# Optimization experiments

Measured on AMD Instinct MI355X. Metric: run time of the kernel, lower is better.

## Reference

```python
import jax, jax.numpy as jnp
import numpy as np

_EPS = 1e-8

# Stacked Sobel kernels, pre-divided by 8 (matches conv2d(...)/8.0 in torch).
# Shape: (O=2, I=1, 3, 3); channel 0 = sobel_x, channel 1 = sobel_y.
_SOBEL = jnp.stack([
    jnp.array([[-1.0, 0.0, 1.0], [-2.0, 0.0, 2.0], [-1.0, 0.0, 1.0]], jnp.float32),
    jnp.array([[-1.0, -2.0, -1.0], [0.0, 0.0, 0.0], [1.0, 2.0, 1.0]], jnp.float32),
])[:, None, :, :] / 8.0


def setup_inputs() -> dict:
    key = jax.random.key(0)
    k1, k2 = jax.random.split(key)
    B, C, H, W = 64, 1, 512, 512
    pred_dist = jax.random.uniform(k1, (B, C, H, W), dtype=jnp.float32) * 10.0
    reachable = jax.random.uniform(k2, (B, C, H, W), dtype=jnp.float32)
    return {"pred_dist": pred_dist, "reachable": reachable}


def reference(pred_dist, reachable) -> jnp.ndarray:
    # Replicate (edge) padding, as F.pad(..., mode='replicate')
    padded = jnp.pad(pred_dist, ((0, 0), (0, 0), (1, 1), (1, 1)), mode="edge")
    # Single conv with 2 output channels computes grad_x and grad_y together.
    grads = jax.lax.conv_general_dilated(
        padded, _SOBEL.astype(pred_dist.dtype),
        window_strides=(1, 1), padding="VALID",
        dimension_numbers=("NCHW", "OIHW", "NCHW"),
    )  # [B, 2, H, W]
    gx = grads[:, 0:1]
    gy = grads[:, 1:2]
    magnitude = jnp.sqrt(gx * gx + gy * gy + _EPS)
    violation = jnp.abs(magnitude - 1.0)
    mask = (reachable > 0.5).astype(violation.dtype)
    denom = jnp.maximum(mask.sum(), 1.0)
    return (violation * mask).sum() / denom
```

## Files before the change

### kernel.cpp

```cpp
#include <hip/hip_runtime.h>
#include <math.h>

#define HW   512
#define IMG  (512 * 512)
#define NB   64
#define GROUPS_PER_ROW 128
#define TOTAL_GROUPS   (NB * HW * GROUPS_PER_ROW)
#define BLOCK 256
#define NBLOCKS 2048
#define NTHREADS (NBLOCKS * BLOCK)

__global__ __launch_bounds__(BLOCK) void eik_main(const float* __restrict__ pred,
                                                  const float* __restrict__ reach,
                                                  float* __restrict__ partials) {
    float vsum = 0.0f;
    float csum = 0.0f;

    for (int g = blockIdx.x * BLOCK + threadIdx.x; g < TOTAL_GROUPS; g += NTHREADS) {
        const int x0 = (g & (GROUPS_PER_ROW - 1)) << 2;
        const int y  = (g >> 7) & (HW - 1);
        const int b  = g >> 16;

        const float* base = pred + (size_t)b * IMG;
        const float* row0 = base + (size_t)y * HW;
        const float* rowm = base + (size_t)(y > 0      ? y - 1 : 0)      * HW;
        const float* rowp = base + (size_t)(y < HW - 1 ? y + 1 : HW - 1) * HW;

        const float4 cm = *(const float4*)(rowm + x0);
        const float4 c0 = *(const float4*)(row0 + x0);
        const float4 cp = *(const float4*)(rowp + x0);
        const float lm = (x0 == 0)        ? rowm[0]    : rowm[x0 - 1];
        const float l0 = (x0 == 0)        ? row0[0]    : row0[x0 - 1];
        const float lp = (x0 == 0)        ? rowp[0]    : rowp[x0 - 1];
        const float rm = (x0 == HW - 4)   ? rowm[HW-1] : rowm[x0 + 4];
        const float r0 = (x0 == HW - 4)   ? row0[HW-1] : row0[x0 + 4];
        const float rp = (x0 == HW - 4)   ? rowp[HW-1] : rowp[x0 + 4];

        const float wm[6] = {lm, cm.x, cm.y, cm.z, cm.w, rm};
        const float w0[6] = {l0, c0.x, c0.y, c0.z, c0.w, r0};
        const float wp[6] = {lp, cp.x, cp.y, cp.z, cp.w, rp};

        const float4 rch = *(const float4*)(reach + (size_t)b * IMG + (size_t)y * HW + x0);
        const float rv[4] = {rch.x, rch.y, rch.z, rch.w};

#pragma unroll
        for (int i = 0; i < 4; ++i) {
            const float gx = ((wm[i+2] - wm[i]) + 2.0f * (w0[i+2] - w0[i]) + (wp[i+2] - wp[i])) * 0.125f;
            const float gy = ((wp[i]   - wm[i]) + 2.0f * (wp[i+1] - wm[i+1]) + (wp[i+2] - wm[i+2])) * 0.125f;
            const float mag  = sqrtf(gx * gx + gy * gy + 1e-8f);
            const float viol = fabsf(mag - 1.0f);
            const bool  m    = rv[i] > 0.5f;
            vsum += m ? viol : 0.0f;
            csum += m ? 1.0f : 0.0f;
        }
    }

#pragma unroll
    for (int off = 32; off > 0; off >>= 1) {
        vsum += __shfl_down(vsum, off, 64);
        csum += __shfl_down(csum, off, 64);
    }

    __shared__ float sv[BLOCK / 64];
    __shared__ float sc[BLOCK / 64];
    const int lane = threadIdx.x & 63;
    const int wid  = threadIdx.x >> 6;
    if (lane == 0) { sv[wid] = vsum; sc[wid] = csum; }
    __syncthreads();
    if (threadIdx.x == 0) {
        partials[2 * blockIdx.x]     = sv[0] + sv[1] + sv[2] + sv[3];
        partials[2 * blockIdx.x + 1] = sc[0] + sc[1] + sc[2] + sc[3];
    }
}

__global__ __launch_bounds__(BLOCK) void eik_finalize(const float* __restrict__ partials,
                                                      float* __restrict__ out) {
    float v = 0.0f, c = 0.0f;
    for (int i = threadIdx.x; i < NBLOCKS; i += BLOCK) {
        v += partials[2 * i];
        c += partials[2 * i + 1];
    }
#pragma unroll
    for (int off = 32; off > 0; off >>= 1) {
        v += __shfl_down(v, off, 64);
        c += __shfl_down(c, off, 64);
    }
    __shared__ float sv[BLOCK / 64];
    __shared__ float sc[BLOCK / 64];
    const int lane = threadIdx.x & 63;
    const int wid  = threadIdx.x >> 6;
    if (lane == 0) { sv[wid] = v; sc[wid] = c; }
    __syncthreads();
    if (threadIdx.x == 0) {
        const float vt = sv[0] + sv[1] + sv[2] + sv[3];
        const float ct = sc[0] + sc[1] + sc[2] + sc[3];
        out[0] = vt / fmaxf(ct, 1.0f);
    }
}

extern "C" void kernel_launch(void* const* d_in, const int* in_sizes, int n_in,
                              void* d_out, int out_size, void* d_ws, size_t ws_size,
                              hipStream_t stream) {
    const float* pred  = (const float*)d_in[0];
    const float* reach = (const float*)d_in[1];
    float* out = (float*)d_out;
    float* ws  = (float*)d_ws;

    eik_main<<<NBLOCKS, BLOCK, 0, stream>>>(pred, reach, ws);
    eik_finalize<<<1, BLOCK, 0, stream>>>(ws, out);
}
```

Measured before the change: 150.6 us.

## Use wave-per-row-strip sliding window with shuffle halos for Sobel stencil

Each 64-lane wave now owns a full 512-wide row and walks down a strip of 8 rows. It keeps three row windows in registers and loads only one new row per step. Horizontal halo values come from lane shuffles instead of extra scalar global loads, which removes the redundant 3x row reloads and the 6 unaligned scalar loads per thread. In exchange, the grid becomes 1024 non-persistent blocks, and halo rows are reloaded at strip boundaries.

```diff
diff --git a/kernel.cpp b/kernel.cpp
--- a/kernel.cpp
+++ b/kernel.cpp
@@ -4,47 +4,64 @@
 #define HW   512
 #define IMG  (512 * 512)
 #define NB   64
-#define GROUPS_PER_ROW 128
-#define TOTAL_GROUPS   (NB * HW * GROUPS_PER_ROW)
+#define T    8
 #define BLOCK 256
-#define NBLOCKS 2048
-#define NTHREADS (NBLOCKS * BLOCK)
+#define WAVES_PER_IMG (HW / T)
+#define TOTAL_WAVES   (NB * WAVES_PER_IMG)
+#define NBLOCKS       (TOTAL_WAVES / (BLOCK / 64))
+
+__device__ __forceinline__ void load_row(const float* __restrict__ prow, int r, int lane,
+                                         float4& q0, float4& q1) {
+    const float* p = prow + (size_t)r * HW + (lane << 3);
+    q0 = *(const float4*)p;
+    q1 = *(const float4*)(p + 4);
+}
+
+__device__ __forceinline__ void make_window(const float4& q0, const float4& q1, int lane,
+                                            float* w) {
+    float lft = __shfl_up(q1.w, 1, 64);
+    float rgt = __shfl_down(q0.x, 1, 64);
+    if (lane == 0)  lft = q0.x;
+    if (lane == 63) rgt = q1.w;
+    w[0] = lft;  w[1] = q0.x; w[2] = q0.y; w[3] = q0.z; w[4] = q0.w;
+    w[5] = q1.x; w[6] = q1.y; w[7] = q1.z; w[8] = q1.w; w[9] = rgt;
+}
 
 __global__ __launch_bounds__(BLOCK) void eik_main(const float* __restrict__ pred,
                                                   const float* __restrict__ reach,
                                                   float* __restrict__ partials) {
-    float vsum = 0.0f;
-    float csum = 0.0f;
+    const int lane = threadIdx.x & 63;
+    const int wave = blockIdx.x * (BLOCK / 64) + (threadIdx.x >> 6);
+    const int b    = wave >> 6;
+    const int y0   = (wave & (WAVES_PER_IMG - 1)) * T;
 
-    for (int g = blockIdx.x * BLOCK + threadIdx.x; g < TOTAL_GROUPS; g += NTHREADS) {
-        const int x0 = (g & (GROUPS_PER_ROW - 1)) << 2;
-        const int y  = (g >> 7) & (HW - 1);
-        const int b  = g >> 16;
+    const float* prow = pred  + (size_t)b * IMG;
+    const float* rrow = reach + (size_t)b * IMG;
 
-        const float* base = pred + (size_t)b * IMG;
-        const float* row0 = base + (size_t)y * HW;
-        const float* rowm = base + (size_t)(y > 0      ? y - 1 : 0)      * HW;
-        const float* rowp = base + (size_t)(y < HW - 1 ? y + 1 : HW - 1) * HW;
+    float wm[10], w0[10], wp[10];
+    float4 a0, a1;
+    load_row(prow, (y0 > 0 ? y0 - 1 : 0), lane, a0, a1);
+    make_window(a0, a1, lane, wm);
+    load_row(prow, y0, lane, a0, a1);
+    make_window(a0, a1, lane, w0);
 
-        const float4 cm = *(const float4*)(rowm + x0);
-        const float4 c0 = *(const float4*)(row0 + x0);
-        const float4 cp = *(const float4*)(rowp + x0);
-        const float lm = (x0 == 0)        ? rowm[0]    : rowm[x0 - 1];
-        const float l0 = (x0 == 0)        ? row0[0]    : row0[x0 - 1];
-        const float lp = (x0 == 0)        ? rowp[0]    : rowp[x0 - 1];
-        const float rm = (x0 == HW - 4)   ? rowm[HW-1] : rowm[x0 + 4];
-        const float r0 = (x0 == HW - 4)   ? row0[HW-1] : row0[x0 + 4];
-        const float rp = (x0 == HW - 4)   ? rowp[HW-1] : rowp[x0 + 4];
-
-        const float wm[6] = {lm, cm.x, cm.y, cm.z, cm.w, rm};
-        const float w0[6] = {l0, c0.x, c0.y, c0.z, c0.w, r0};
-        const float wp[6] = {lp, cp.x, cp.y, cp.z, cp.w, rp};
-
-        const float4 rch = *(const float4*)(reach + (size_t)b * IMG + (size_t)y * HW + x0);
-        const float rv[4] = {rch.x, rch.y, rch.z, rch.w};
+    float vsum = 0.0f, csum = 0.0f;
 
 #pragma unroll
-        for (int i = 0; i < 4; ++i) {
+    for (int t = 0; t < T; ++t) {
+        const int y  = y0 + t;
+        const int yp = (y + 1 < HW) ? y + 1 : HW - 1;
+        load_row(prow, yp, lane, a0, a1);
+
+        const float* rp = rrow + (size_t)y * HW + (lane << 3);
+        const float4 r0 = *(const float4*)rp;
+        const float4 r1 = *(const float4*)(rp + 4);
+
+        make_window(a0, a1, lane, wp);
+
+        const float rv[8] = {r0.x, r0.y, r0.z, r0.w, r1.x, r1.y, r1.z, r1.w};
+#pragma unroll
+        for (int i = 0; i < 8; ++i) {
             const float gx = ((wm[i+2] - wm[i]) + 2.0f * (w0[i+2] - w0[i]) + (wp[i+2] - wp[i])) * 0.125f;
             const float gy = ((wp[i]   - wm[i]) + 2.0f * (wp[i+1] - wm[i+1]) + (wp[i+2] - wm[i+2])) * 0.125f;
             const float mag  = sqrtf(gx * gx + gy * gy + 1e-8f);
@@ -53,6 +70,8 @@
             vsum += m ? viol : 0.0f;
             csum += m ? 1.0f : 0.0f;
         }
+#pragma unroll
+        for (int i = 0; i < 10; ++i) { wm[i] = w0[i]; w0[i] = wp[i]; }
     }
 
 #pragma unroll
@@ -63,8 +82,7 @@
 
     __shared__ float sv[BLOCK / 64];
     __shared__ float sc[BLOCK / 64];
-    const int lane = threadIdx.x & 63;
-    const int wid  = threadIdx.x >> 6;
+    const int wid = threadIdx.x >> 6;
     if (lane == 0) { sv[wid] = vsum; sc[wid] = csum; }
     __syncthreads();
     if (threadIdx.x == 0) {
```

New measurement: 148.1 us. Within noise of the previous version (-1.7%).

## Map one wave per row and share halos via lane shuffles

Applied to the files above, without the earlier changes.

Each wavefront now processes a full image row with 8 pixels per lane, loading them as two float4 vectors per input row. Left and right neighbours are exchanged with shuffle instructions instead of separate scalar global loads. The Sobel stencil is split into separable vertical sums and differences, which cuts arithmetic. The grid grows to one block per four rows, so finalize reduces more partials and the workspace must be larger.

```diff
diff --git a/kernel.cpp b/kernel.cpp
--- a/kernel.cpp
+++ b/kernel.cpp
@@ -4,55 +4,69 @@
 #define HW   512
 #define IMG  (512 * 512)
 #define NB   64
-#define GROUPS_PER_ROW 128
-#define TOTAL_GROUPS   (NB * HW * GROUPS_PER_ROW)
 #define BLOCK 256
-#define NBLOCKS 2048
-#define NTHREADS (NBLOCKS * BLOCK)
+#define WAVES_PER_BLOCK (BLOCK / 64)
+#define TOTAL_ROWS (NB * HW)
+#define NBLOCKS    (TOTAL_ROWS / WAVES_PER_BLOCK)
 
 __global__ __launch_bounds__(BLOCK) void eik_main(const float* __restrict__ pred,
                                                   const float* __restrict__ reach,
                                                   float* __restrict__ partials) {
-    float vsum = 0.0f;
-    float csum = 0.0f;
+    const int lane = threadIdx.x & 63;
+    const int w    = blockIdx.x * WAVES_PER_BLOCK + (threadIdx.x >> 6);
+    const int y    = w & (HW - 1);
+    const int b    = w >> 9;
 
-    for (int g = blockIdx.x * BLOCK + threadIdx.x; g < TOTAL_GROUPS; g += NTHREADS) {
-        const int x0 = (g & (GROUPS_PER_ROW - 1)) << 2;
-        const int y  = (g >> 7) & (HW - 1);
-        const int b  = g >> 16;
+    const int ym = (y > 0)      ? y - 1 : 0;
+    const int yp = (y < HW - 1) ? y + 1 : HW - 1;
 
-        const float* base = pred + (size_t)b * IMG;
-        const float* row0 = base + (size_t)y * HW;
-        const float* rowm = base + (size_t)(y > 0      ? y - 1 : 0)      * HW;
-        const float* rowp = base + (size_t)(y < HW - 1 ? y + 1 : HW - 1) * HW;
+    const float* base = pred + (size_t)b * IMG;
+    const float* pm = base + (size_t)ym * HW + (lane << 3);
+    const float* p0 = base + (size_t)y  * HW + (lane << 3);
+    const float* pp = base + (size_t)yp * HW + (lane << 3);
+    const float* rp = reach + (size_t)b * IMG + (size_t)y * HW + (lane << 3);
 
-        const float4 cm = *(const float4*)(rowm + x0);
-        const float4 c0 = *(const float4*)(row0 + x0);
-        const float4 cp = *(const float4*)(rowp + x0);
-        const float lm = (x0 == 0)        ? rowm[0]    : rowm[x0 - 1];
-        const float l0 = (x0 == 0)        ? row0[0]    : row0[x0 - 1];
-        const float lp = (x0 == 0)        ? rowp[0]    : rowp[x0 - 1];
-        const float rm = (x0 == HW - 4)   ? rowm[HW-1] : rowm[x0 + 4];
-        const float r0 = (x0 == HW - 4)   ? row0[HW-1] : row0[x0 + 4];
-        const float rp = (x0 == HW - 4)   ? rowp[HW-1] : rowp[x0 + 4];
+    const float4 m0 = *(const float4*)pm;
+    const float4 m1 = *(const float4*)(pm + 4);
+    const float4 c0 = *(const float4*)p0;
+    const float4 c1 = *(const float4*)(p0 + 4);
+    const float4 q0 = *(const float4*)pp;
+    const float4 q1 = *(const float4*)(pp + 4);
+    const float4 r0 = *(const float4*)rp;
+    const float4 r1 = *(const float4*)(rp + 4);
 
-        const float wm[6] = {lm, cm.x, cm.y, cm.z, cm.w, rm};
-        const float w0[6] = {l0, c0.x, c0.y, c0.z, c0.w, r0};
-        const float wp[6] = {lp, cp.x, cp.y, cp.z, cp.w, rp};
+    const float am[8] = {m0.x, m0.y, m0.z, m0.w, m1.x, m1.y, m1.z, m1.w};
+    const float a0[8] = {c0.x, c0.y, c0.z, c0.w, c1.x, c1.y, c1.z, c1.w};
+    const float ap[8] = {q0.x, q0.y, q0.z, q0.w, q1.x, q1.y, q1.z, q1.w};
+    const float rv[8] = {r0.x, r0.y, r0.z, r0.w, r1.x, r1.y, r1.z, r1.w};
 
-        const float4 rch = *(const float4*)(reach + (size_t)b * IMG + (size_t)y * HW + x0);
-        const float rv[4] = {rch.x, rch.y, rch.z, rch.w};
+    float s[8], d[8];
+#pragma unroll
+    for (int i = 0; i < 8; ++i) {
+        s[i] = am[i] + 2.0f * a0[i] + ap[i];
+        d[i] = ap[i] - am[i];
+    }
 
+    float sl = __shfl_up(s[7], 1, 64);
+    float dl = __shfl_up(d[7], 1, 64);
+    float sr = __shfl_down(s[0], 1, 64);
+    float dr = __shfl_down(d[0], 1, 64);
+    if (lane == 0)  { sl = s[0]; dl = d[0]; }
+    if (lane == 63) { sr = s[7]; dr = d[7]; }
+
+    const float S[10] = {sl, s[0], s[1], s[2], s[3], s[4], s[5], s[6], s[7], sr};
+    const float D[10] = {dl, d[0], d[1], d[2], d[3], d[4], d[5], d[6], d[7], dr};
+
+    float vsum = 0.0f, csum = 0.0f;
 #pragma unroll
-        for (int i = 0; i < 4; ++i) {
-            const float gx = ((wm[i+2] - wm[i]) + 2.0f * (w0[i+2] - w0[i]) + (wp[i+2] - wp[i])) * 0.125f;
-            const float gy = ((wp[i]   - wm[i]) + 2.0f * (wp[i+1] - wm[i+1]) + (wp[i+2] - wm[i+2])) * 0.125f;
-            const float mag  = sqrtf(gx * gx + gy * gy + 1e-8f);
-            const float viol = fabsf(mag - 1.0f);
-            const bool  m    = rv[i] > 0.5f;
-            vsum += m ? viol : 0.0f;
-            csum += m ? 1.0f : 0.0f;
-        }
+    for (int i = 0; i < 8; ++i) {
+        const float gx = (S[i+2] - S[i]) * 0.125f;
+        const float gy = (D[i] + 2.0f * D[i+1] + D[i+2]) * 0.125f;
+        const float mag  = sqrtf(gx * gx + gy * gy + 1e-8f);
+        const float viol = fabsf(mag - 1.0f);
+        const bool  m    = rv[i] > 0.5f;
+        vsum += m ? viol : 0.0f;
+        csum += m ? 1.0f : 0.0f;
     }
 
 #pragma unroll
@@ -61,10 +75,9 @@
         csum += __shfl_down(csum, off, 64);
     }
 
-    __shared__ float sv[BLOCK / 64];
-    __shared__ float sc[BLOCK / 64];
-    const int lane = threadIdx.x & 63;
-    const int wid  = threadIdx.x >> 6;
+    __shared__ float sv[WAVES_PER_BLOCK];
+    __shared__ float sc[WAVES_PER_BLOCK];
+    const int wid = threadIdx.x >> 6;
     if (lane == 0) { sv[wid] = vsum; sc[wid] = csum; }
     __syncthreads();
     if (threadIdx.x == 0) {
@@ -85,8 +98,8 @@
         v += __shfl_down(v, off, 64);
         c += __shfl_down(c, off, 64);
     }
-    __shared__ float sv[BLOCK / 64];
-    __shared__ float sc[BLOCK / 64];
+    __shared__ float sv[WAVES_PER_BLOCK];
+    __shared__ float sc[WAVES_PER_BLOCK];
     const int lane = threadIdx.x & 63;
     const int wid  = threadIdx.x >> 6;
     if (lane == 0) { sv[wid] = v; sc[wid] = c; }
```

Measured after the change: 150.0 us. No clear change (-0.4%).
